# Kernel optimization log

Measured on AMD Instinct MI355X. Metric: run time of the kernel, lower is better.

The kernel has to match this reference:

```python
import jax, jax.numpy as jnp
import numpy as np

N_NODES = 70000
N_EDGES = 2_000_000
IN_CH, FEAT_CH, OUT_CH = 1044, 128, 3


def _gcn_norm(src_sl, dst_sl, n_nodes, dtype):
    # PyG gcn_norm with add_self_loops=True, edge_weight=1:
    # deg over target nodes, norm = deg^-1/2[src] * deg^-1/2[dst]
    deg = jax.ops.segment_sum(jnp.ones(src_sl.shape[0], dtype=dtype), dst_sl,
                              num_segments=n_nodes)
    dinv = jnp.where(deg > 0, jax.lax.rsqrt(deg), jnp.zeros((), dtype))
    return dinv[src_sl] * dinv[dst_sl]


def _gcn_layer(x, src_sl, dst_sl, norm, W, b, n_nodes):
    h = x @ W                                  # [N, out] linear transform first
    msg = h[src_sl] * norm[:, None]            # gather + scale
    out = jax.ops.segment_sum(msg, dst_sl, num_segments=n_nodes)  # scatter-add
    return out + b


def setup_inputs() -> dict:
    key = jax.random.key(0)
    ks = jax.random.split(key, 6)
    features = jax.random.normal(ks[0], (N_NODES, IN_CH), dtype=jnp.float32)
    edges = jax.random.randint(ks[1], (2, N_EDGES), 0, N_NODES, dtype=jnp.int64)
    edges2 = jax.random.randint(ks[2], (2, N_EDGES), 0, N_NODES, dtype=jnp.int64)
    edge_features = jax.random.normal(ks[3], (N_EDGES,), dtype=jnp.float32)
    W1 = jax.random.normal(ks[4], (IN_CH, FEAT_CH), dtype=jnp.float32) * (1.0 / np.sqrt(IN_CH))
    b1 = jnp.zeros((FEAT_CH,), dtype=jnp.float32)
    W2 = jax.random.normal(ks[5], (FEAT_CH, OUT_CH), dtype=jnp.float32) * (1.0 / np.sqrt(FEAT_CH))
    b2 = jnp.zeros((OUT_CH,), dtype=jnp.float32)
    return {"features": features, "edges": edges, "edges2": edges2,
            "edge_features": edge_features, "W1": W1, "b1": b1, "W2": W2, "b2": b2}


def reference(features, edges, edges2, edge_features, W1, b1, W2, b2):
    # edge_features is discarded by the module (set to None); edges2 unused.
    n = features.shape[0]
    loop = jnp.arange(n, dtype=edges.dtype)
    src_sl = jnp.concatenate([edges[0], loop])  # self-loops appended
    dst_sl = jnp.concatenate([edges[1], loop])
    norm = _gcn_norm(src_sl, dst_sl, n, features.dtype)
    x = _gcn_layer(features, src_sl, dst_sl, norm, W1, b1, n)
    x = jax.nn.relu(x)
    # dropout is identity in eval mode (deterministic reference)
    return _gcn_layer(x, src_sl, dst_sl, norm, W2, b2, n)
```

## Files before the change

### kernel.cpp

```cpp
#include <hip/hip_runtime.h>
#include <hip/hip_bf16.h>

#define K_IN   1044
#define N_FEAT 128
#define KPAD   1056
#define LDA    40
#define NSTEP  (KPAD / 32)
#define BM     96

#define NB     512
#define BWMAX  256
#define EPB    8192

typedef __attribute__((ext_vector_type(8))) short short8;
typedef __attribute__((ext_vector_type(4))) float f32x4;

__device__ __forceinline__ ushort f2bf(float f) {
  unsigned x = __float_as_uint(f);
  x += 0x7fffu + ((x >> 16) & 1u);
  return (ushort)(x >> 16);
}
__device__ __forceinline__ uint pkbf(float lo, float hi) {
  __hip_bfloat162 h = __float22bfloat162_rn(make_float2(lo, hi));
  return *reinterpret_cast<uint*>(&h);
}
__device__ __forceinline__ float bflo(uint v) { return __uint_as_float(v << 16); }
__device__ __forceinline__ float bfhi(uint v) { return __uint_as_float(v & 0xFFFF0000u); }


__global__ __launch_bounds__(256) void csr_hist_kernel(const int* __restrict__ dst,
                                                       int* __restrict__ bt, int E, int bw) {
  __shared__ int h[NB];
  const int t = threadIdx.x;
  for (int i = t; i < NB; i += 256) h[i] = 0;
  __syncthreads();
  const int e0 = blockIdx.x * EPB;
  const int e1 = min(e0 + EPB, E);
  for (int e = e0 + t; e < e1; e += 256) atomicAdd(&h[dst[e] / bw], 1);
  __syncthreads();
  for (int i = t; i < NB; i += 256)
    if (h[i]) atomicAdd(&bt[i], h[i]);
}

__global__ __launch_bounds__(256) void csr_bucket_scan_kernel(const int* __restrict__ bt,
                                                              int* __restrict__ bucket_base,
                                                              int* __restrict__ bucket_cursor) {
  __shared__ int sc[256];
  const int t = threadIdx.x;
  int v0 = bt[2 * t], v1 = bt[2 * t + 1];
  int s = v0 + v1;
  sc[t] = s;
  __syncthreads();
  for (int off = 1; off < 256; off <<= 1) {
    int x = (t >= off) ? sc[t - off] : 0;
    __syncthreads();
    sc[t] += x;
    __syncthreads();
  }
  int excl = sc[t] - s;
  bucket_base[2 * t]     = excl;
  bucket_base[2 * t + 1] = excl + v0;
  bucket_cursor[2 * t]     = excl;
  bucket_cursor[2 * t + 1] = excl + v0;
  if (t == 255) bucket_base[NB] = sc[255];
}

__global__ __launch_bounds__(256) void csr_stage_kernel(const int* __restrict__ src,
                                                        const int* __restrict__ dst,
                                                        int* __restrict__ bucket_cursor,
                                                        uint2* __restrict__ staging, int E, int bw) {
  __shared__ int h[NB];
  __shared__ int cur[NB];
  const int t = threadIdx.x;
  for (int i = t; i < NB; i += 256) h[i] = 0;
  __syncthreads();
  const int e0 = blockIdx.x * EPB;
  const int e1 = min(e0 + EPB, E);
  for (int e = e0 + t; e < e1; e += 256) atomicAdd(&h[dst[e] / bw], 1);
  __syncthreads();
  for (int i = t; i < NB; i += 256)
    cur[i] = h[i] ? atomicAdd(&bucket_cursor[i], h[i]) : 0;
  __syncthreads();
  for (int e = e0 + t; e < e1; e += 256) {
    int d = dst[e];
    int p = atomicAdd(&cur[d / bw], 1);
    staging[p] = make_uint2((uint)src[e], (uint)d);
  }
}

__global__ __launch_bounds__(256) void csr_final_kernel(const uint2* __restrict__ staging,
                                                        const int* __restrict__ bucket_base,
                                                        int* __restrict__ row_ptr,
                                                        int* __restrict__ sorted_src,
                                                        float* __restrict__ dinv,
                                                        int N, int bw, int E) {
  __shared__ int hist[BWMAX];
  __shared__ int sc[256];
  const int b = blockIdx.x;
  const int t = threadIdx.x;
  if (b == 0 && t == 0) row_ptr[N] = E;
  const int node0 = b * bw;
  const int nn = min(bw, N - node0);
  if (nn <= 0) return;
  const int base = bucket_base[b];
  const int cnt  = bucket_base[b + 1] - base;

  for (int i = t; i < BWMAX; i += 256) hist[i] = 0;
  __syncthreads();
  for (int i = t; i < cnt; i += 256) {
    uint2 p = staging[base + i];
    atomicAdd(&hist[(int)p.y - node0], 1);
  }
  __syncthreads();
  int v = (t < nn) ? hist[t] : 0;
  if (t < nn) dinv[node0 + t] = rsqrtf((float)(v + 1));
  sc[t] = v;
  __syncthreads();
  for (int off = 1; off < 256; off <<= 1) {
    int x = (t >= off) ? sc[t - off] : 0;
    __syncthreads();
    sc[t] += x;
    __syncthreads();
  }
  int excl = sc[t] - v;
  if (t < nn) row_ptr[node0 + t] = base + excl;
  if (t < nn) hist[t] = excl;
  __syncthreads();
  for (int i = t; i < cnt; i += 256) {
    uint2 p = staging[base + i];
    int c = atomicAdd(&hist[(int)p.y - node0], 1);
    sorted_src[base + c] = (int)p.x;
  }
}


__global__ void convert_w1_kernel(const float* __restrict__ W1, ushort* __restrict__ W1T) {
  int idx = blockIdx.x * blockDim.x + threadIdx.x;
  if (idx >= N_FEAT * KPAD) return;
  int c = idx / KPAD, k = idx - c * KPAD;
  W1T[idx] = (k < K_IN) ? f2bf(W1[(size_t)k * N_FEAT + c]) : (ushort)0;
}


__global__ __launch_bounds__(256) void gemm1_mfma_kernel(const float* __restrict__ X,
                                                         const ushort* __restrict__ W1T,
                                                         const float* __restrict__ dinv,
                                                         ushort* __restrict__ G1, int M) {
  __shared__ ushort Asb[2][BM * LDA];
  __shared__ ushort Bsb[2][128 * LDA];

  const int t = threadIdx.x;
  const int row0 = blockIdx.x * BM;

  const int ar0 = t >> 3;
  const int ak4 = (t & 7) * 4;
  const int br = t >> 1;
  const int bk = (t & 1) * 16;

  const float*  aptr = X + (size_t)row0 * K_IN;
  const ushort* bptr = W1T + (size_t)br * KPAD;

  const int l = t & 63;
  const int wid = t >> 6;
  const int wm = wid >> 1, wn = wid & 1;
  const int lr = l & 15;
  const int lko = (l >> 4) * 8;

  f32x4 acc[3][4] = {};

  float4 pa[3];
  uint4 pb0, pb1;

  auto load_step = [&](int s) {
    const int kk = s * 32;
    const int gk = kk + ak4;
    #pragma unroll
    for (int i = 0; i < 3; i++) {
      const int row = ar0 + i * 32;
      const bool rv = (row0 + row) < M;
      if (rv && gk + 4 <= K_IN) {
        pa[i] = *(const float4*)(aptr + (size_t)row * K_IN + gk);
      } else {
        float tmp[4];
        #pragma unroll
        for (int j = 0; j < 4; j++)
          tmp[j] = (rv && gk + j < K_IN) ? aptr[(size_t)row * K_IN + gk + j] : 0.f;
        pa[i] = make_float4(tmp[0], tmp[1], tmp[2], tmp[3]);
      }
    }
    const uint4* q = (const uint4*)(bptr + kk + bk);
    pb0 = q[0]; pb1 = q[1];
  };
  auto store_step = [&](int buf) {
    #pragma unroll
    for (int i = 0; i < 3; i++) {
      uint w0 = pkbf(pa[i].x, pa[i].y), w1 = pkbf(pa[i].z, pa[i].w);
      *(uint2*)&Asb[buf][(ar0 + i * 32) * LDA + ak4] = make_uint2(w0, w1);
    }
    *(uint4*)&Bsb[buf][br * LDA + bk]     = pb0;
    *(uint4*)&Bsb[buf][br * LDA + bk + 8] = pb1;
  };

  load_step(0);
  store_step(0);
  __syncthreads();

  #pragma unroll 1
  for (int s = 0; s < NSTEP; s++) {
    const int cur = s & 1;
    if (s + 1 < NSTEP) load_step(s + 1);

    short8 af[3], bfr[4];
    #pragma unroll
    for (int m = 0; m < 3; m++)
      af[m] = *(const short8*)&Asb[cur][(wm * 48 + m * 16 + lr) * LDA + lko];
    #pragma unroll
    for (int n = 0; n < 4; n++)
      bfr[n] = *(const short8*)&Bsb[cur][(wn * 64 + n * 16 + lr) * LDA + lko];

    #pragma unroll
    for (int m = 0; m < 3; m++)
      #pragma unroll
      for (int n = 0; n < 4; n++)
        acc[m][n] = __builtin_amdgcn_mfma_f32_16x16x32_bf16(af[m], bfr[n], acc[m][n], 0, 0, 0);

    if (s + 1 < NSTEP) store_step(cur ^ 1);
    __syncthreads();
  }

  const int rbase = row0 + wm * 48 + (l >> 4) * 4;
  const int cbase = wn * 64 + lr;
  #pragma unroll
  for (int m = 0; m < 3; m++) {
    #pragma unroll
    for (int r = 0; r < 4; r++) {
      int row = rbase + m * 16 + r;
      if (row < M) {
        float dv = dinv[row];
        #pragma unroll
        for (int n = 0; n < 4; n++)
          G1[(size_t)row * N_FEAT + cbase + n * 16] = f2bf(dv * acc[m][n][r]);
      }
    }
  }
}


__global__ __launch_bounds__(256) void agg1mm_kernel(const ushort* __restrict__ G1,
                                                     const int* __restrict__ row_ptr,
                                                     const int* __restrict__ sorted_src,
                                                     const float* __restrict__ dinv,
                                                     const float* __restrict__ b1,
                                                     const float* __restrict__ W2,
                                                     float* __restrict__ G2, int N) {
  const int w = (blockIdx.x * blockDim.x + threadIdx.x) >> 6;
  const int lane = threadIdx.x & 63;
  if (w >= N) return;
  const int beg = row_ptr[w], end = row_ptr[w + 1];
  const uint* g1u = (const uint*)G1;
  const int co = lane;

  uint vs = g1u[((size_t)w << 6) + co];
  float a0 = bflo(vs), a1 = bfhi(vs);

  int e = beg;
  for (; e + 8 <= end; e += 8) {
    int s[8];
    #pragma unroll
    for (int i = 0; i < 8; i++) s[i] = sorted_src[e + i];
    #pragma unroll
    for (int i = 0; i < 8; i++) {
      uint v = g1u[((size_t)s[i] << 6) + co];
      a0 += bflo(v); a1 += bfhi(v);
    }
  }
  for (; e < end; e++) {
    uint v = g1u[((size_t)sorted_src[e] << 6) + co];
    a0 += bflo(v); a1 += bfhi(v);
  }

  const float di = dinv[w];
  float r0 = fmaxf(fmaf(di, a0, b1[2 * co + 0]), 0.f);
  float r1 = fmaxf(fmaf(di, a1, b1[2 * co + 1]), 0.f);

  const float* wrow = W2 + 6 * co;
  float s0 = r0 * wrow[0] + r1 * wrow[3];
  float s1 = r0 * wrow[1] + r1 * wrow[4];
  float s2 = r0 * wrow[2] + r1 * wrow[5];
  #pragma unroll
  for (int off = 32; off > 0; off >>= 1) {
    s0 += __shfl_down(s0, off);
    s1 += __shfl_down(s1, off);
    s2 += __shfl_down(s2, off);
  }
  if (lane == 0) {
    G2[w * 3 + 0] = di * s0;
    G2[w * 3 + 1] = di * s1;
    G2[w * 3 + 2] = di * s2;
  }
}


__global__ __launch_bounds__(256) void agg2_kernel(const float* __restrict__ G2,
                                                   const int* __restrict__ row_ptr,
                                                   const int* __restrict__ sorted_src,
                                                   const float* __restrict__ dinv,
                                                   const float* __restrict__ b2,
                                                   float* __restrict__ out, int N) {
  int t = blockIdx.x * blockDim.x + threadIdx.x;
  int node = t >> 6, lane = t & 63;
  if (node >= N) return;
  int beg = row_ptr[node], end = row_ptr[node + 1];
  float a0 = 0.f, a1 = 0.f, a2 = 0.f;
  for (int e = beg + lane; e < end; e += 64) {
    int s = sorted_src[e];
    a0 += G2[s * 3 + 0];
    a1 += G2[s * 3 + 1];
    a2 += G2[s * 3 + 2];
  }
  #pragma unroll
  for (int off = 32; off > 0; off >>= 1) {
    a0 += __shfl_down(a0, off);
    a1 += __shfl_down(a1, off);
    a2 += __shfl_down(a2, off);
  }
  if (lane == 0) {
    float di = dinv[node];
    out[node * 3 + 0] = di * (a0 + G2[node * 3 + 0]) + b2[0];
    out[node * 3 + 1] = di * (a1 + G2[node * 3 + 1]) + b2[1];
    out[node * 3 + 2] = di * (a2 + G2[node * 3 + 2]) + b2[2];
  }
}


extern "C" void kernel_launch(void* const* d_in, const int* in_sizes, int n_in,
                              void* d_out, int out_size, void* d_ws, size_t ws_size,
                              hipStream_t stream) {
  const float* features = (const float*)d_in[0];
  const int*   edges    = (const int*)d_in[1];
  const float* W1 = (const float*)d_in[4];
  const float* b1 = (const float*)d_in[5];
  const float* W2 = (const float*)d_in[6];
  const float* b2 = (const float*)d_in[7];
  float* out = (float*)d_out;

  const int N = in_sizes[0] / K_IN;
  const int E = in_sizes[1] / 2;
  const int* src = edges;
  const int* dst = edges + E;
  const int bw = (N + NB - 1) / NB;

  char* ws = (char*)d_ws;
  size_t off = 0;
  auto alloc = [&](size_t bytes) {
    void* p = ws + off;
    off += (bytes + 255) & ~(size_t)255;
    return p;
  };
  int*    bt            = (int*)   alloc((size_t)NB * sizeof(int));
  int*    bucket_base   = (int*)   alloc((size_t)(NB + 1) * sizeof(int));
  int*    bucket_cursor = (int*)   alloc((size_t)NB * sizeof(int));
  int*    row_ptr       = (int*)   alloc((size_t)(N + 1) * sizeof(int));
  float*  dinv          = (float*) alloc((size_t)N * sizeof(float));
  uint2*  staging       = (uint2*) alloc((size_t)E * sizeof(uint2));
  int*    sorted_src    = (int*)   alloc((size_t)E * sizeof(int));
  ushort* G1            = (ushort*)alloc((size_t)N * N_FEAT * sizeof(ushort));
  float*  G2            = (float*) alloc((size_t)N * 3 * sizeof(float));
  ushort* W1T           = (ushort*)alloc((size_t)N_FEAT * KPAD * sizeof(ushort));
  (void)ws_size;

  const int eblocks = (E + EPB - 1) / EPB;

  hipMemsetAsync(bt, 0, (size_t)NB * sizeof(int), stream);
  convert_w1_kernel<<<(N_FEAT * KPAD + 255) / 256, 256, 0, stream>>>(W1, W1T);
  csr_hist_kernel<<<eblocks, 256, 0, stream>>>(dst, bt, E, bw);
  csr_bucket_scan_kernel<<<1, 256, 0, stream>>>(bt, bucket_base, bucket_cursor);
  csr_stage_kernel<<<eblocks, 256, 0, stream>>>(src, dst, bucket_cursor, staging, E, bw);
  csr_final_kernel<<<NB, 256, 0, stream>>>(staging, bucket_base, row_ptr, sorted_src, dinv, N, bw, E);
  gemm1_mfma_kernel<<<(N + BM - 1) / BM, 256, 0, stream>>>(features, W1T, dinv, G1, N);
  agg1mm_kernel<<<((size_t)N * 64 + 255) / 256, 256, 0, stream>>>(G1, row_ptr, sorted_src, dinv, b1, W2, G2, N);
  agg2_kernel<<<((size_t)N * 64 + 255) / 256, 256, 0, stream>>>(G2, row_ptr, sorted_src, dinv, b2, out, N);
}
```

Baseline: 266.6 us.

## Load GEMM tiles directly into LDS with XOR swizzle and pack CSR staging

The first GEMM now stages A (fp32 features) and B (bf16 W1T) with global_load_lds 16-byte loads straight into LDS, skipping the register round-trip. Conversion of A to bf16 moves to the fragment read. Both tiles use XOR-swizzled layouts to avoid bank conflicts, and W1T is pre-swizzled on conversion to match. Separately, CSR staging entries shrink from two 32-bit words to one by packing the source index with the node offset within its bucket, halving staging traffic. The trade-offs are doubled LDS for the fp32 A tile, clamped out-of-range loads that rely on zero-padded weights, and an assumption that node ids fit in 24 bits and bucket widths in 8 bits.

```diff
diff --git a/kernel.cpp b/kernel.cpp
--- a/kernel.cpp
+++ b/kernel.cpp
@@ -4,7 +4,6 @@
 #define K_IN   1044
 #define N_FEAT 128
 #define KPAD   1056
-#define LDA    40
 #define NSTEP  (KPAD / 32)
 #define BM     96
 
@@ -26,6 +25,12 @@
 }
 __device__ __forceinline__ float bflo(uint v) { return __uint_as_float(v << 16); }
 __device__ __forceinline__ float bfhi(uint v) { return __uint_as_float(v & 0xFFFF0000u); }
+
+__device__ __forceinline__ void gld16(const void* g, void* l) {
+  __builtin_amdgcn_global_load_lds(
+      (const __attribute__((address_space(1))) unsigned int*)g,
+      (__attribute__((address_space(3))) unsigned int*)l, 16, 0, 0);
+}
 
 
 __global__ __launch_bounds__(256) void csr_hist_kernel(const int* __restrict__ dst,
@@ -68,7 +73,7 @@
 __global__ __launch_bounds__(256) void csr_stage_kernel(const int* __restrict__ src,
                                                         const int* __restrict__ dst,
                                                         int* __restrict__ bucket_cursor,
-                                                        uint2* __restrict__ staging, int E, int bw) {
+                                                        uint* __restrict__ staging, int E, int bw) {
   __shared__ int h[NB];
   __shared__ int cur[NB];
   const int t = threadIdx.x;
@@ -83,12 +88,13 @@
   __syncthreads();
   for (int e = e0 + t; e < e1; e += 256) {
     int d = dst[e];
-    int p = atomicAdd(&cur[d / bw], 1);
-    staging[p] = make_uint2((uint)src[e], (uint)d);
-  }
-}
-
-__global__ __launch_bounds__(256) void csr_final_kernel(const uint2* __restrict__ staging,
+    int b = d / bw;
+    int p = atomicAdd(&cur[b], 1);
+    staging[p] = ((uint)src[e] << 8) | (uint)(d - b * bw);
+  }
+}
+
+__global__ __launch_bounds__(256) void csr_final_kernel(const uint* __restrict__ staging,
                                                         const int* __restrict__ bucket_base,
                                                         int* __restrict__ row_ptr,
                                                         int* __restrict__ sorted_src,
@@ -107,10 +113,8 @@
 
   for (int i = t; i < BWMAX; i += 256) hist[i] = 0;
   __syncthreads();
-  for (int i = t; i < cnt; i += 256) {
-    uint2 p = staging[base + i];
-    atomicAdd(&hist[(int)p.y - node0], 1);
-  }
+  for (int i = t; i < cnt; i += 256)
+    atomicAdd(&hist[staging[base + i] & 255u], 1);
   __syncthreads();
   int v = (t < nn) ? hist[t] : 0;
   if (t < nn) dinv[node0 + t] = rsqrtf((float)(v + 1));
@@ -127,9 +131,9 @@
   if (t < nn) hist[t] = excl;
   __syncthreads();
   for (int i = t; i < cnt; i += 256) {
-    uint2 p = staging[base + i];
-    int c = atomicAdd(&hist[(int)p.y - node0], 1);
-    sorted_src[base + c] = (int)p.x;
+    uint p = staging[base + i];
+    int c = atomicAdd(&hist[p & 255u], 1);
+    sorted_src[base + c] = (int)(p >> 8);
   }
 }
 
@@ -137,8 +141,13 @@
 __global__ void convert_w1_kernel(const float* __restrict__ W1, ushort* __restrict__ W1T) {
   int idx = blockIdx.x * blockDim.x + threadIdx.x;
   if (idx >= N_FEAT * KPAD) return;
-  int c = idx / KPAD, k = idx - c * KPAD;
-  W1T[idx] = (k < K_IN) ? f2bf(W1[(size_t)k * N_FEAT + c]) : (ushort)0;
+  int col = idx / KPAD, k = idx - col * KPAD;
+  int kk = k & ~31;
+  int jp = (k >> 3) & 3;
+  int e  = k & 7;
+  int jl = jp ^ (col & 3);
+  int ksrc = kk + 8 * jl + e;
+  W1T[idx] = (ksrc < K_IN) ? f2bf(W1[(size_t)ksrc * N_FEAT + col]) : (ushort)0;
 }
 
 
@@ -146,77 +155,60 @@
                                                          const ushort* __restrict__ W1T,
                                                          const float* __restrict__ dinv,
                                                          ushort* __restrict__ G1, int M) {
-  __shared__ ushort Asb[2][BM * LDA];
-  __shared__ ushort Bsb[2][128 * LDA];
+  __shared__ float  Af[2][BM * 32];
+  __shared__ ushort Bsb[2][128 * 32];
 
   const int t = threadIdx.x;
   const int row0 = blockIdx.x * BM;
-
-  const int ar0 = t >> 3;
-  const int ak4 = (t & 7) * 4;
-  const int br = t >> 1;
-  const int bk = (t & 1) * 16;
-
-  const float*  aptr = X + (size_t)row0 * K_IN;
-  const ushort* bptr = W1T + (size_t)br * KPAD;
-
-  const int l = t & 63;
-  const int wid = t >> 6;
-  const int wm = wid >> 1, wn = wid & 1;
-  const int lr = l & 15;
-  const int lko = (l >> 4) * 8;
+  const int w = t >> 6, l = t & 63;
+  const int w24 = w * 24, w32 = w * 32;
+  const int Mm1 = M - 1;
+
+  const int wm = w >> 1, wn = w & 1;
+  const int lr = l & 15, g = l >> 4;
+  const int k7 = lr & 7, k3 = lr & 3;
 
   f32x4 acc[3][4] = {};
 
-  float4 pa[3];
-  uint4 pb0, pb1;
-
-  auto load_step = [&](int s) {
+  auto stage = [&](int s, int buf) {
     const int kk = s * 32;
-    const int gk = kk + ak4;
     #pragma unroll
     for (int i = 0; i < 3; i++) {
-      const int row = ar0 + i * 32;
-      const bool rv = (row0 + row) < M;
-      if (rv && gk + 4 <= K_IN) {
-        pa[i] = *(const float4*)(aptr + (size_t)row * K_IN + gk);
-      } else {
-        float tmp[4];
-        #pragma unroll
-        for (int j = 0; j < 4; j++)
-          tmp[j] = (rv && gk + j < K_IN) ? aptr[(size_t)row * K_IN + gk + j] : 0.f;
-        pa[i] = make_float4(tmp[0], tmp[1], tmp[2], tmp[3]);
-      }
-    }
-    const uint4* q = (const uint4*)(bptr + kk + bk);
-    pb0 = q[0]; pb1 = q[1];
+      int r  = w24 + i * 8 + (l >> 3);
+      int jl = (l & 7) ^ (r & 7);
+      int grow = min(row0 + r, Mm1);
+      int gk   = min(kk + 4 * jl, K_IN - 4);
+      gld16(X + (size_t)grow * K_IN + gk, (void*)&Af[buf][(w24 + i * 8) * 32]);
+    }
+    #pragma unroll
+    for (int i = 0; i < 2; i++) {
+      int r = w32 + i * 16 + (l >> 2);
+      gld16(W1T + (size_t)r * KPAD + kk + 8 * (l & 3),
+            (void*)&Bsb[buf][(w32 + i * 16) * 32]);
+    }
   };
-  auto store_step = [&](int buf) {
-    #pragma unroll
-    for (int i = 0; i < 3; i++) {
-      uint w0 = pkbf(pa[i].x, pa[i].y), w1 = pkbf(pa[i].z, pa[i].w);
-      *(uint2*)&Asb[buf][(ar0 + i * 32) * LDA + ak4] = make_uint2(w0, w1);
-    }
-    *(uint4*)&Bsb[buf][br * LDA + bk]     = pb0;
-    *(uint4*)&Bsb[buf][br * LDA + bk + 8] = pb1;
-  };
-
-  load_step(0);
-  store_step(0);
-  __syncthreads();
-
+
+  stage(0, 0);
+  __syncthreads();
+
+  int cur = 0;
   #pragma unroll 1
   for (int s = 0; s < NSTEP; s++) {
-    const int cur = s & 1;
-    if (s + 1 < NSTEP) load_step(s + 1);
+    if (s + 1 < NSTEP) stage(s + 1, cur ^ 1);
 
     short8 af[3], bfr[4];
     #pragma unroll
-    for (int m = 0; m < 3; m++)
-      af[m] = *(const short8*)&Asb[cur][(wm * 48 + m * 16 + lr) * LDA + lko];
+    for (int m = 0; m < 3; m++) {
+      const float* rp = &Af[cur][(wm * 48 + m * 16 + lr) * 32];
+      float4 a0 = *(const float4*)&rp[((2 * g + 0) ^ k7) << 2];
+      float4 a1 = *(const float4*)&rp[((2 * g + 1) ^ k7) << 2];
+      uint4 uu = make_uint4(pkbf(a0.x, a0.y), pkbf(a0.z, a0.w),
+                            pkbf(a1.x, a1.y), pkbf(a1.z, a1.w));
+      af[m] = *(short8*)&uu;
+    }
     #pragma unroll
     for (int n = 0; n < 4; n++)
-      bfr[n] = *(const short8*)&Bsb[cur][(wn * 64 + n * 16 + lr) * LDA + lko];
+      bfr[n] = *(const short8*)&Bsb[cur][(wn * 64 + n * 16 + lr) * 32 + ((g ^ k3) << 3)];
 
     #pragma unroll
     for (int m = 0; m < 3; m++)
@@ -224,8 +216,8 @@
       for (int n = 0; n < 4; n++)
         acc[m][n] = __builtin_amdgcn_mfma_f32_16x16x32_bf16(af[m], bfr[n], acc[m][n], 0, 0, 0);
 
-    if (s + 1 < NSTEP) store_step(cur ^ 1);
-    __syncthreads();
+    __syncthreads();
+    cur ^= 1;
   }
 
   const int rbase = row0 + wm * 48 + (l >> 4) * 4;
@@ -362,7 +354,7 @@
   int*    bucket_cursor = (int*)   alloc((size_t)NB * sizeof(int));
   int*    row_ptr       = (int*)   alloc((size_t)(N + 1) * sizeof(int));
   float*  dinv          = (float*) alloc((size_t)N * sizeof(float));
-  uint2*  staging       = (uint2*) alloc((size_t)E * sizeof(uint2));
+  uint*   staging       = (uint*)  alloc((size_t)E * sizeof(uint));
   int*    sorted_src    = (int*)   alloc((size_t)E * sizeof(int));
   ushort* G1            = (ushort*)alloc((size_t)N * N_FEAT * sizeof(ushort));
   float*  G2            = (float*) alloc((size_t)N * 3 * sizeof(float));
```

Result: faster. 259.8 us (-2.6%).
